# Kernel tuning notes

Measured on AMD Instinct MI355X. Metric: run time of the kernel, lower is better.

Reference implementation:

```python
import jax, jax.numpy as jnp
import numpy as np
import math

T, P, L, C, H, NPTS = 243, 17, 4, 128, 8, 4
DH = C // H


def _ln(x, g, b):
    m = jnp.mean(x, axis=-1, keepdims=True)
    v = jnp.mean((x - m) ** 2, axis=-1, keepdims=True)
    return (x - m) * jax.lax.rsqrt(v + 1e-5) * g + b


def _bilinear(v, grid):
    # v: [B, D, Hh, Ww]; grid: [B, Q, Pt, 2] in [-1,1], (x->W, y->H),
    # align_corners=False, zero padding (matches F.grid_sample in MSDeformAttn core)
    B, D, Hh, Ww = v.shape
    x = (grid[..., 0] + 1.0) * (Ww * 0.5) - 0.5
    y = (grid[..., 1] + 1.0) * (Hh * 0.5) - 0.5
    x0 = jnp.floor(x)
    y0 = jnp.floor(y)
    x0i = x0.astype(jnp.int32)
    y0i = y0.astype(jnp.int32)
    x1i = x0i + 1
    y1i = y0i + 1
    wx1 = x - x0
    wx0 = 1.0 - wx1
    wy1 = y - y0
    wy0 = 1.0 - wy1
    vf = v.reshape(B, D, Hh * Ww)
    Q, Pt = x.shape[1], x.shape[2]

    def gather(yi, xi):
        valid = ((yi >= 0) & (yi < Hh) & (xi >= 0) & (xi < Ww)).astype(v.dtype)
        idx = jnp.clip(yi, 0, Hh - 1) * Ww + jnp.clip(xi, 0, Ww - 1)
        g = jnp.take_along_axis(vf, idx.reshape(B, 1, Q * Pt), axis=2).reshape(B, D, Q, Pt)
        return g * valid[:, None]

    return (gather(y0i, x0i) * (wy0 * wx0)[:, None]
            + gather(y0i, x1i) * (wy0 * wx1)[:, None]
            + gather(y1i, x0i) * (wy1 * wx0)[:, None]
            + gather(y1i, x1i) * (wy1 * wx1)[:, None])  # [B, D, Q, Pt]


def _forward(x, ref_points, pe_buf, learn_pos, w_off, b_off, w_attn, b_attn,
             w_val, b_val, w_out, b_out, in_w, in_b, out_w, out_b,
             fc1_w, fc1_b, fc2_w, fc2_b, g1, be1, g2, be2, g3, be3):
    b, t, p, l, c = x.shape  # l = n_levels + 1
    Lq = t * p * L
    x0 = x[..., :1, :]
    xs = x[..., 1:, :].reshape(b, Lq, c)
    # --- subforward_self: norm_1 -> PE(query) -> MSDeformAttn ---
    xn = _ln(xs, g1, be1)
    q = (xn.reshape(b, t, p, L, c) + pe_buf + learn_pos).reshape(b, Lq, c)
    off = (q @ w_off.T + b_off).reshape(b, Lq, H, L, NPTS, 2)
    aw = jax.nn.softmax((q @ w_attn.T + b_attn).reshape(b, Lq, H, L * NPTS), axis=-1)
    aw = aw.reshape(b, Lq, H, L, NPTS)
    ref = jnp.broadcast_to(ref_points[:, :, :, None, :], (b, t, p, L, 2)).reshape(b, Lq, 2)
    normalizer = jnp.array([p, t], dtype=x.dtype)  # (W, H) per level
    loc = ref[:, :, None, None, None, :] + off / normalizer  # [b,Lq,H,L,Pt,2]
    grids = 2.0 * loc - 1.0
    val = (xn @ w_val.T + b_val).reshape(b, t, p, L, H, DH)
    v_maps = val.transpose(3, 0, 4, 5, 1, 2).reshape(L, b * H, DH, t, p)
    g = grids.transpose(3, 0, 2, 1, 4, 5).reshape(L, b * H, Lq, NPTS, 2)
    sampled = jax.vmap(_bilinear)(v_maps, g)  # [L, b*H, DH, Lq, Pt]
    aw_t = aw.transpose(3, 0, 2, 1, 4).reshape(L, b * H, 1, Lq, NPTS)
    o = jnp.sum(sampled * aw_t, axis=(0, 4))  # [b*H, DH, Lq]
    o = o.reshape(b, H, DH, Lq).transpose(0, 3, 1, 2).reshape(b, Lq, c)
    xs = (o @ w_out.T + b_out) + xs
    # --- concat level-0 back, cross (self) MHA over (p*l) tokens per frame ---
    xcat = jnp.concatenate([x0, xs.reshape(b, t, p, L, c)], axis=3).reshape(b * t, p * l, c)
    xn2 = _ln(xcat, g2, be2)
    qkv = xn2 @ in_w.T + in_b
    qh, kh, vh = jnp.split(qkv, 3, axis=-1)
    S = p * l
    qh = qh.reshape(b * t, S, H, DH)
    kh = kh.reshape(b * t, S, H, DH)
    vh = vh.reshape(b * t, S, H, DH)
    att = jax.nn.softmax(jnp.einsum('bqhd,bkhd->bhqk', qh, kh) / math.sqrt(DH), axis=-1)
    ca = jnp.einsum('bhqk,bkhd->bqhd', att, vh).reshape(b * t, S, c) @ out_w.T + out_b
    xcat = ca + xcat
    xr = xcat.reshape(b, t, p, l, c)
    # --- MLP block ---
    h = _ln(xr, g3, be3)
    h = jax.nn.gelu(h @ fc1_w.T + fc1_b, approximate=False) @ fc2_w.T + fc2_b
    return h + xr


def setup_inputs() -> dict:
    key = jax.random.key(0)
    ks = jax.random.split(key, 20)
    B = 2
    s = 0.02
    x = jax.random.normal(ks[0], (B, T, P, L + 1, C), jnp.float32)
    ref_points = jax.random.uniform(ks[1], (B, T, P, 2), dtype=jnp.float32)
    # sinusoidal PE buffer
    pos = np.arange(T, dtype=np.float32)[:, None]
    div = np.exp(np.arange(0, C, 2, dtype=np.float32) * (-math.log(10000.0) / C))
    ang = pos * div  # [T, C//2]
    pe = np.zeros((1, T, P, L, C), np.float32)
    pe[..., 0::2] = np.sin(ang)[None, :, None, None, :]
    pe[..., 1::2] = np.cos(ang)[None, :, None, None, :]
    rn = lambda k, shp: s * jax.random.normal(k, shp, jnp.float32)
    return {
        'x': x, 'ref_points': ref_points,
        'pe_buf': jnp.asarray(pe),
        'learn_pos': rn(ks[2], (1, T, P, L, C)),
        'w_off': rn(ks[3], (H * L * NPTS * 2, C)), 'b_off': rn(ks[4], (H * L * NPTS * 2,)),
        'w_attn': rn(ks[5], (H * L * NPTS, C)), 'b_attn': rn(ks[6], (H * L * NPTS,)),
        'w_val': rn(ks[7], (C, C)), 'b_val': rn(ks[8], (C,)),
        'w_out': rn(ks[9], (C, C)), 'b_out': rn(ks[10], (C,)),
        'in_w': rn(ks[11], (3 * C, C)), 'in_b': rn(ks[12], (3 * C,)),
        'out_w': rn(ks[13], (C, C)), 'out_b': rn(ks[14], (C,)),
        'fc1_w': rn(ks[15], (4 * C, C)), 'fc1_b': rn(ks[16], (4 * C,)),
        'fc2_w': rn(ks[17], (C, 4 * C)), 'fc2_b': rn(ks[18], (C,)),
        'g1': jnp.ones((C,), jnp.float32), 'be1': jnp.zeros((C,), jnp.float32),
        'g2': jnp.ones((C,), jnp.float32), 'be2': jnp.zeros((C,), jnp.float32),
        'g3': jnp.ones((C,), jnp.float32), 'be3': jnp.zeros((C,), jnp.float32),
    }


def reference(x, ref_points, pe_buf, learn_pos, w_off, b_off, w_attn, b_attn,
              w_val, b_val, w_out, b_out, in_w, in_b, out_w, out_b,
              fc1_w, fc1_b, fc2_w, fc2_b, g1, be1, g2, be2, g3, be3):
    return _forward(x, ref_points, pe_buf, learn_pos, w_off, b_off, w_attn, b_attn,
                    w_val, b_val, w_out, b_out, in_w, in_b, out_w, out_b,
                    fc1_w, fc1_b, fc2_w, fc2_b, g1, be1, g2, be2, g3, be3)
```

## Files before the change

### kernel.cpp

```cpp
#include <hip/hip_runtime.h>
#include <math.h>

#define T_ 243
#define P_ 17
#define L_ 4
#define C_ 128
#define H_ 8
#define NPTS_ 4
#define DH_ 16
#define B_ 2
#define LQ (T_*P_*L_)
#define NT1 (B_*LQ)
#define LL (L_+1)
#define S_ (P_*LL)
#define NT2 (B_*T_*P_*LL)

typedef __attribute__((ext_vector_type(8))) short short8v;
typedef __attribute__((ext_vector_type(4))) short short4v;
typedef __attribute__((ext_vector_type(4))) float float4v;

__device__ __forceinline__ unsigned short f2bf(float f){
  union { float f; unsigned u; } un; un.f = f;
  unsigned r = un.u + 0x7FFF + ((un.u >> 16) & 1);
  return (unsigned short)(r >> 16);
}
__device__ __forceinline__ float bf2f(unsigned short u){
  union { unsigned u; float f; } un; un.u = ((unsigned)u) << 16; return un.f;
}
__device__ __forceinline__ void dma16(const unsigned short* g, unsigned short* l){
  __builtin_amdgcn_global_load_lds(
      (const __attribute__((address_space(1))) void*)g,
      (__attribute__((address_space(3))) void*)l, 16, 0, 0);
}

__global__ void k_wcvt(const float* __restrict__ w0, const float* __restrict__ w1,
                       const float* __restrict__ w2, const float* __restrict__ w3,
                       const float* __restrict__ w4, const float* __restrict__ w5,
                       const float* __restrict__ w6, const float* __restrict__ w7,
                       unsigned short* __restrict__ dst){
  int i = blockIdx.x*256 + threadIdx.x;
  if (i >= 278528) return;
  float v;
  if      (i < 32768)  v = w0[i];
  else if (i < 49152)  v = w1[i-32768];
  else if (i < 65536)  v = w2[i-49152];
  else if (i < 81920)  v = w3[i-65536];
  else if (i < 131072) v = w4[i-81920];
  else if (i < 147456) v = w5[i-131072];
  else if (i < 212992) v = w6[i-147456];
  else                 v = w7[i-212992];
  dst[i] = f2bf(v);
}

__global__ __launch_bounds__(256) void k_ln1_q(
    const float* __restrict__ x, const float* __restrict__ pe,
    const float* __restrict__ lpos, const float* __restrict__ g1,
    const float* __restrict__ be1, const float* __restrict__ g2,
    const float* __restrict__ be2, unsigned short* __restrict__ xn,
    unsigned short* __restrict__ q, float* __restrict__ xcat,
    unsigned short* __restrict__ xn2) {
  int w = threadIdx.x >> 6; int lane = threadIdx.x & 63;
  int i = blockIdx.x*4 + w;
  int c = lane*2;
  if (i < NT1){
    int b = i / LQ; int r = i % LQ;
    int t = r / (P_*L_); int rp = r % (P_*L_);
    int p = rp / L_; int lv = rp % L_;
    const float* xrow = x + (((size_t)(b*T_+t)*P_ + p)*LL + 1 + lv)*C_;
    float2 v = *(const float2*)(xrow + c);
    float s1 = v.x + v.y, s2 = v.x*v.x + v.y*v.y;
    #pragma unroll
    for (int d=1; d<64; d<<=1){ s1 += __shfl_xor(s1,d); s2 += __shfl_xor(s2,d); }
    float mean = s1*(1.0f/C_);
    float var  = s2*(1.0f/C_) - mean*mean;
    float inv = rsqrtf(var + 1e-5f);
    float2 gg = *(const float2*)(g1 + c);
    float2 bb = *(const float2*)(be1 + c);
    float xn0 = (v.x - mean)*inv*gg.x + bb.x;
    float xn1 = (v.y - mean)*inv*gg.y + bb.y;
    size_t oi = (size_t)i*C_ + c;
    *(unsigned*)(xn + oi) = (unsigned)f2bf(xn0) | ((unsigned)f2bf(xn1) << 16);
    size_t pidx = (((size_t)t*P_ + p)*L_ + lv)*C_ + c;
    float2 pv = *(const float2*)(pe + pidx);
    float2 lp = *(const float2*)(lpos + pidx);
    *(unsigned*)(q + oi) = (unsigned)f2bf(xn0 + pv.x + lp.x) | ((unsigned)f2bf(xn1 + pv.y + lp.y) << 16);
  } else {
    int i0 = i - NT1;
    if (i0 >= B_*T_*P_) return;
    size_t xrow = (size_t)i0*LL;
    const float* xr = x + xrow*C_;
    float2 v = *(const float2*)(xr + c);
    float s1 = v.x + v.y, s2 = v.x*v.x + v.y*v.y;
    #pragma unroll
    for (int d=1; d<64; d<<=1){ s1 += __shfl_xor(s1,d); s2 += __shfl_xor(s2,d); }
    float mean = s1*(1.0f/C_);
    float var  = s2*(1.0f/C_) - mean*mean;
    float inv = rsqrtf(var + 1e-5f);
    float2 gg = *(const float2*)(g2 + c);
    float2 bb = *(const float2*)(be2 + c);
    *(float2*)(xcat + xrow*C_ + c) = v;
    float o0 = (v.x - mean)*inv*gg.x + bb.x;
    float o1 = (v.y - mean)*inv*gg.y + bb.y;
    *(unsigned*)(xn2 + xrow*C_ + c) = (unsigned)f2bf(o0) | ((unsigned)f2bf(o1) << 16);
  }
}

template<int K, int N, int EPI>
__global__ __launch_bounds__(256) void k_mm(
    const unsigned short* __restrict__ A, const unsigned short* __restrict__ Bw,
    const float* __restrict__ bias, const float* __restrict__ res,
    float* __restrict__ outF, unsigned short* __restrict__ outB,
    const float* __restrict__ xres, const float* __restrict__ lng,
    const float* __restrict__ lnbe, int M)
{
  constexpr int NST = K / 128;
  __shared__ unsigned short As[64*128];
  __shared__ unsigned short Bs[128*128];
  int tid = threadIdx.x;
  int lane = tid & 63;
  int w = tid >> 6;
  int lr = lane & 15, kg = lane >> 4;
  int m0 = blockIdx.x * 64;
  int n0 = blockIdx.y * 128;
  int lrow = lane >> 4;
  int lch  = lane & 15;
  float4v acc[8] = {};
  for (int st = 0; st < NST; ++st){
    int kk = st*128;
    if (st) __syncthreads();
    #pragma unroll
    for (int j = 0; j < 4; ++j){
      int rb = w*16 + j*4;
      int srcch = lch ^ ((rb + lrow) & 7);
      dma16(A + (size_t)(m0 + rb + lrow)*K + kk + srcch*8, As + rb*128);
    }
    #pragma unroll
    for (int j = 0; j < 8; ++j){
      int rb = w*32 + j*4;
      int srcch = lch ^ ((rb + lrow) & 7);
      dma16(Bw + (size_t)(n0 + rb + lrow)*K + kk + srcch*8, Bs + rb*128);
    }
    __syncthreads();
    #pragma unroll
    for (int ks = 0; ks < 4; ++ks){
      int cn = ks*4 + kg;
      int arow = w*16 + lr;
      short8v af = *(const short8v*)(As + arow*128 + ((cn ^ (arow & 7)) * 8));
      #pragma unroll
      for (int nf = 0; nf < 8; ++nf){
        int brow = nf*16 + lr;
        short8v bf = *(const short8v*)(Bs + brow*128 + ((cn ^ (brow & 7)) * 8));
        acc[nf] = __builtin_amdgcn_mfma_f32_16x16x32_bf16(af, bf, acc[nf], 0, 0, 0);
      }
    }
  }
  #pragma unroll
  for (int j = 0; j < 4; ++j){
    int gr = m0 + w*16 + kg*4 + j;
    if (gr >= M) continue;
    if (EPI == 3 || EPI == 4 || EPI == 5){
      #pragma unroll
      for (int nf = 0; nf < 8; ++nf){
        int gc = n0 + nf*16 + lr;
        float v = acc[nf][j] + bias[gc];
        if (EPI == 3) {
          outF[(size_t)gr*N + gc] = v + res[(size_t)gr*N + gc];
        } else if (EPI == 4) {
          float gv = 0.5f*v*(1.0f + erff(v*0.70710678118654752440f));
          outB[(size_t)gr*N + gc] = f2bf(gv);
        } else {
          outB[(size_t)gr*N + gc] = f2bf(v);
        }
      }
    } else {
      size_t xrow;
      if (EPI == 6){
        int b = gr / LQ; int r = gr % LQ;
        int t = r / (P_*L_); int rp = r % (P_*L_);
        int p = rp / L_; int lv = rp % L_;
        xrow = (((size_t)(b*T_+t)*P_ + p)*LL) + 1 + lv;
      } else {
        xrow = (size_t)gr;
      }
      float vals[8];
      float s = 0.f, sq = 0.f;
      #pragma unroll
      for (int nf = 0; nf < 8; ++nf){
        int gc = n0 + nf*16 + lr;
        float v = acc[nf][j] + bias[gc];
        if (EPI == 6) v += xres[xrow*C_ + gc];
        else          v += res[xrow*C_ + gc];
        vals[nf] = v; s += v; sq += v*v;
      }
      #pragma unroll
      for (int d = 1; d < 16; d <<= 1){ s += __shfl_xor(s, d); sq += __shfl_xor(sq, d); }
      float mean = s*(1.0f/128.f);
      float varr = sq*(1.0f/128.f) - mean*mean;
      float linv = rsqrtf(varr + 1e-5f);
      #pragma unroll
      for (int nf = 0; nf < 8; ++nf){
        int gc = n0 + nf*16 + lr;
        outF[xrow*C_ + gc] = vals[nf];
        float ln = (vals[nf] - mean)*linv*lng[gc] + lnbe[gc];
        outB[xrow*C_ + gc] = f2bf(ln);
      }
    }
  }
}

__global__ __launch_bounds__(256) void k_mm3(
    const unsigned short* __restrict__ Aq, const unsigned short* __restrict__ Axn,
    const unsigned short* __restrict__ Bw,
    const float* __restrict__ b_off, const float* __restrict__ b_attn,
    const float* __restrict__ b_val,
    unsigned short* __restrict__ off_b, unsigned short* __restrict__ aw_b,
    unsigned short* __restrict__ vm_b, int M)
{
  __shared__ unsigned short As[64*128];
  __shared__ unsigned short Bs[128*128];
  int tid = threadIdx.x;
  int lane = tid & 63;
  int w = tid >> 6;
  int lr = lane & 15, kg = lane >> 4;
  int m0 = blockIdx.x * 64;
  int y  = blockIdx.y;
  int n0 = y * 128;
  const unsigned short* A = (y == 3) ? Axn : Aq;
  int lrow = lane >> 4;
  int lch  = lane & 15;
  float4v acc[8] = {};
  #pragma unroll
  for (int j = 0; j < 4; ++j){
    int rb = w*16 + j*4;
    int srcch = lch ^ ((rb + lrow) & 7);
    dma16(A + (size_t)(m0 + rb + lrow)*128 + srcch*8, As + rb*128);
  }
  #pragma unroll
  for (int j = 0; j < 8; ++j){
    int rb = w*32 + j*4;
    int srcch = lch ^ ((rb + lrow) & 7);
    dma16(Bw + (size_t)(n0 + rb + lrow)*128 + srcch*8, Bs + rb*128);
  }
  __syncthreads();
  #pragma unroll
  for (int ks = 0; ks < 4; ++ks){
    int cn = ks*4 + kg;
    int arow = w*16 + lr;
    short8v af = *(const short8v*)(As + arow*128 + ((cn ^ (arow & 7)) * 8));
    #pragma unroll
    for (int nf = 0; nf < 8; ++nf){
      int brow = nf*16 + lr;
      short8v bf = *(const short8v*)(Bs + brow*128 + ((cn ^ (brow & 7)) * 8));
      acc[nf] = __builtin_amdgcn_mfma_f32_16x16x32_bf16(af, bf, acc[nf], 0, 0, 0);
    }
  }
  const float* bias = (y < 2) ? b_off : (y == 2 ? b_attn - 256 : b_val - 384);
  #pragma unroll
  for (int j = 0; j < 4; ++j){
    int gr = m0 + w*16 + kg*4 + j;
    if (gr >= M) continue;
    #pragma unroll
    for (int nf = 0; nf < 8; ++nf){
      int gc = n0 + nf*16 + lr;
      float v = acc[nf][j] + bias[gc];
      unsigned short bv = f2bf(v);
      if (y < 2)      off_b[(size_t)gr*256 + gc]       = bv;
      else if (y==2)  aw_b [(size_t)gr*128 + gc - 256] = bv;
      else            vm_b [(size_t)gr*128 + gc - 384] = bv;
    }
  }
}

__global__ __launch_bounds__(256) void k_sample(
    const unsigned short* __restrict__ off, const unsigned short* __restrict__ awl,
    const float* __restrict__ refp, const unsigned short* __restrict__ vmap,
    unsigned short* __restrict__ o){
  int gid = blockIdx.x*256 + threadIdx.x;
  if (gid >= NT1*H_) return;
  int h = gid & 7; int i = gid >> 3;
  int b = i / LQ; int r = i % LQ;
  int t = r/(P_*L_); int rp = r%(P_*L_); int p = rp/L_;
  size_t rpi = (((size_t)b*T_+t)*P_+p)*2;
  float refx = refp[rpi + 0]*P_ - 0.5f;
  float refy = refp[rpi + 1]*T_ - 0.5f;

  float offv[32];
  {
    const short8v* op8 = (const short8v*)(off + (size_t)i*256 + h*32);
    #pragma unroll
    for (int s=0;s<4;++s){ short8v v = op8[s];
      #pragma unroll
      for (int j=0;j<8;++j) offv[s*8+j] = bf2f((unsigned short)v[j]); }
  }
  float awv[16];
  {
    const short8v* ap8 = (const short8v*)(awl + (size_t)i*128 + h*16);
    #pragma unroll
    for (int s=0;s<2;++s){ short8v v = ap8[s];
      #pragma unroll
      for (int j=0;j<8;++j) awv[s*8+j] = bf2f((unsigned short)v[j]); }
  }
  float m = awv[0];
  #pragma unroll
  for (int k=1;k<16;++k) m = fmaxf(m, awv[k]);
  float sum = 0.f;
  #pragma unroll
  for (int k=0;k<16;++k){ awv[k] = __expf(awv[k]-m); sum += awv[k]; }
  float inv = 1.f/sum;
  #pragma unroll
  for (int k=0;k<16;++k) awv[k] *= inv;

  float acc[16];
  #pragma unroll
  for (int d=0;d<16;++d) acc[d]=0.f;

  #pragma unroll
  for (int lv=0; lv<L_; ++lv){
    const unsigned short* vlv = vmap + ((size_t)b*LQ + lv)*128 + h*16;
    #pragma unroll
    for (int pt=0; pt<NPTS_; ++pt){
      float px = refx + offv[(lv*4+pt)*2+0];
      float py = refy + offv[(lv*4+pt)*2+1];
      float w  = awv[lv*4+pt];
      float fx = floorf(px), fy = floorf(py);
      int x0 = (int)fx, y0 = (int)fy;
      float wx1 = px - fx, wx0 = 1.f - wx1;
      float wy1 = py - fy, wy0 = 1.f - wy1;
      float cw[4] = {w*wy0*wx0, w*wy0*wx1, w*wy1*wx0, w*wy1*wx1};
      int ys[4] = {y0, y0, y0+1, y0+1};
      int xs[4] = {x0, x0+1, x0, x0+1};
      #pragma unroll
      for (int cidx=0; cidx<4; ++cidx){
        int yy = ys[cidx], xx = xs[cidx];
        if (yy>=0 && yy<T_ && xx>=0 && xx<P_){
          const short8v* vp = (const short8v*)(vlv + (size_t)(yy*P_ + xx)*(L_*128));
          short8v v0 = vp[0], v1 = vp[1];
          float wgt = cw[cidx];
          #pragma unroll
          for (int d=0;d<8;++d){
            acc[d]   = fmaf(wgt, bf2f((unsigned short)v0[d]), acc[d]);
            acc[8+d] = fmaf(wgt, bf2f((unsigned short)v1[d]), acc[8+d]);
          }
        }
      }
    }
  }
  short8v o0, o1;
  #pragma unroll
  for (int d=0;d<8;++d){ o0[d] = (short)f2bf(acc[d]); o1[d] = (short)f2bf(acc[8+d]); }
  short8v* op = (short8v*)(o + (size_t)i*C_ + h*DH_);
  op[0] = o0; op[1] = o1;
}

#define AT6_WAVE 6976
__global__ __launch_bounds__(128) void k_attn6(const unsigned short* __restrict__ qkv,
                                               unsigned short* __restrict__ ca){
  __shared__ unsigned short alds[2*AT6_WAVE];
  int w = threadIdx.x >> 6; int lane = threadIdx.x & 63;
  int bt = blockIdx.x >> 2; int hp = blockIdx.x & 3;
  int h = hp*2 + w;
  unsigned short* Kb  = alds + w*AT6_WAVE;
  unsigned short* Vb  = Kb + 1920;
  unsigned short* Pb0 = Kb + 3648;
  unsigned short* Pb1 = Kb + 5312;
  const unsigned short* base = qkv + (size_t)bt*85*384 + h*16;
  for (int idx = lane; idx < 192; idx += 64){
    int s = idx >> 1; int d0 = (idx & 1)*8;
    short8v kv = {}, vv = {};
    if (s < 85){
      const unsigned short* rp = base + (size_t)s*384 + d0;
      kv = *(const short8v*)(rp + 128);
      vv = *(const short8v*)(rp + 256);
    }
    *(short8v*)(Kb + s*20 + d0) = kv;
    #pragma unroll
    for (int j=0;j<8;++j) Vb[(d0+j)*108 + s] = (unsigned short)vv[j];
  }
  __syncthreads();
  int g = lane >> 4; int li = lane & 15;
  const short8v zero8 = {};
  short8v qf0 = zero8, qf1 = zero8;
  if (g < 2){
    if (li < 85) qf0 = *(const short8v*)(base + (size_t)li*384 + g*8);
    int q1i = 16 + li;
    if (q1i < 85) qf1 = *(const short8v*)(base + (size_t)q1i*384 + g*8);
  }
  #pragma unroll 1
  for (int qp = 0; qp < 3; ++qp){
    short8v qn0 = zero8, qn1 = zero8;
    if (qp < 2 && g < 2){
      int a = (qp+1)*32 + li, b2 = a + 16;
      if (a  < 85) qn0 = *(const short8v*)(base + (size_t)a *384 + g*8);
      if (b2 < 85) qn1 = *(const short8v*)(base + (size_t)b2*384 + g*8);
    }
    float4v sc0[6], sc1[6];
    __builtin_amdgcn_s_setprio(1);
    #pragma unroll
    for (int kt = 0; kt < 6; ++kt){
      short8v kf = zero8;
      if (g < 2) kf = *(const short8v*)(Kb + (kt*16 + li)*20 + g*8);
      float4v z = {};
      sc0[kt] = __builtin_amdgcn_mfma_f32_16x16x32_bf16(kf, qf0, z, 0, 0, 0);
      sc1[kt] = __builtin_amdgcn_mfma_f32_16x16x32_bf16(kf, qf1, z, 0, 0, 0);
    }
    __builtin_amdgcn_s_setprio(0);
    float m0 = -1e30f, m1 = -1e30f;
    #pragma unroll
    for (int kt = 0; kt < 6; ++kt)
      #pragma unroll
      for (int j = 0; j < 4; ++j){
        bool msk = (kt == 5 && (g*4 + j) >= 5);
        float v0 = sc0[kt][j]*0.25f; if (msk) v0 = -1e30f;
        float v1 = sc1[kt][j]*0.25f; if (msk) v1 = -1e30f;
        sc0[kt][j] = v0; m0 = fmaxf(m0, v0);
        sc1[kt][j] = v1; m1 = fmaxf(m1, v1);
      }
    m0 = fmaxf(m0, __shfl_xor(m0, 16)); m1 = fmaxf(m1, __shfl_xor(m1, 16));
    m0 = fmaxf(m0, __shfl_xor(m0, 32)); m1 = fmaxf(m1, __shfl_xor(m1, 32));
    float sum0 = 0.f, sum1 = 0.f;
    #pragma unroll
    for (int kt = 0; kt < 6; ++kt){
      short4v p0, p1;
      #pragma unroll
      for (int j = 0; j < 4; ++j){
        float e0 = __expf(sc0[kt][j] - m0); sum0 += e0; p0[j] = (short)f2bf(e0);
        float e1 = __expf(sc1[kt][j] - m1); sum1 += e1; p1[j] = (short)f2bf(e1);
      }
      *(short4v*)(Pb0 + li*104 + kt*16 + g*4) = p0;
      *(short4v*)(Pb1 + li*104 + kt*16 + g*4) = p1;
    }
    sum0 += __shfl_xor(sum0, 16); sum1 += __shfl_xor(sum1, 16);
    sum0 += __shfl_xor(sum0, 32); sum1 += __shfl_xor(sum1, 32);
    float inv0 = 1.f/sum0, inv1 = 1.f/sum1;
    float4v o0 = {}, o1 = {};
    __builtin_amdgcn_s_setprio(1);
    #pragma unroll
    for (int kt32 = 0; kt32 < 3; ++kt32){
      short8v vf  = *(const short8v*)(Vb  + li*108 + kt32*32 + g*8);
      short8v p80 = *(const short8v*)(Pb0 + li*104 + kt32*32 + g*8);
      short8v p81 = *(const short8v*)(Pb1 + li*104 + kt32*32 + g*8);
      o0 = __builtin_amdgcn_mfma_f32_16x16x32_bf16(vf, p80, o0, 0, 0, 0);
      o1 = __builtin_amdgcn_mfma_f32_16x16x32_bf16(vf, p81, o1, 0, 0, 0);
    }
    __builtin_amdgcn_s_setprio(0);
    int q0 = qp*32 + li, q1 = q0 + 16;
    if (q0 < 85){
      short4v ov;
      #pragma unroll
      for (int j=0;j<4;++j) ov[j] = (short)f2bf(o0[j]*inv0);
      *(short4v*)(ca + ((size_t)bt*85 + q0)*128 + h*16 + g*4) = ov;
    }
    if (q1 < 85){
      short4v ov;
      #pragma unroll
      for (int j=0;j<4;++j) ov[j] = (short)f2bf(o1[j]*inv1);
      *(short4v*)(ca + ((size_t)bt*85 + q1)*128 + h*16 + g*4) = ov;
    }
    qf0 = qn0; qf1 = qn1;
  }
}

extern "C" void kernel_launch(void* const* d_in, const int* in_sizes, int n_in,
                              void* d_out, int out_size, void* d_ws, size_t ws_size,
                              hipStream_t stream) {
  (void)in_sizes; (void)n_in; (void)out_size; (void)ws_size;
  const float* x      = (const float*)d_in[0];
  const float* refp   = (const float*)d_in[1];
  const float* pe     = (const float*)d_in[2];
  const float* lpos   = (const float*)d_in[3];
  const float* w_off  = (const float*)d_in[4];
  const float* b_off  = (const float*)d_in[5];
  const float* w_attn = (const float*)d_in[6];
  const float* b_attn = (const float*)d_in[7];
  const float* w_val  = (const float*)d_in[8];
  const float* b_val  = (const float*)d_in[9];
  const float* w_out  = (const float*)d_in[10];
  const float* b_out  = (const float*)d_in[11];
  const float* in_w   = (const float*)d_in[12];
  const float* in_b   = (const float*)d_in[13];
  const float* out_w  = (const float*)d_in[14];
  const float* out_b  = (const float*)d_in[15];
  const float* fc1_w  = (const float*)d_in[16];
  const float* fc1_b  = (const float*)d_in[17];
  const float* fc2_w  = (const float*)d_in[18];
  const float* fc2_b  = (const float*)d_in[19];
  const float* g1     = (const float*)d_in[20];
  const float* be1    = (const float*)d_in[21];
  const float* g2     = (const float*)d_in[22];
  const float* be2    = (const float*)d_in[23];
  const float* g3     = (const float*)d_in[24];
  const float* be3    = (const float*)d_in[25];
  float* out = (float*)d_out;
  char* wsb = (char*)d_ws;

  unsigned short* xn_b  = (unsigned short*)(wsb + 0);
  unsigned short* q_b   = (unsigned short*)(wsb + 8460288);
  unsigned short* off_b = (unsigned short*)(wsb + 16920576);
  unsigned short* aw_b  = (unsigned short*)(wsb + 33841152);
  unsigned short* vm_b  = (unsigned short*)(wsb + 42301440);
  unsigned short* o_b   = (unsigned short*)(wsb + 50761728);
  float*          xcatB = (float*)(wsb + 59222016);
  unsigned short* xn2_b = (unsigned short*)(wsb + 80372736);
  unsigned short* qkv_b = (unsigned short*)(wsb + 90948096);
  unsigned short* wb    = (unsigned short*)(wsb + 122674176);
  unsigned short* ca_b  = (unsigned short*)(wsb + 0);
  unsigned short* ln3_b = (unsigned short*)(wsb + 80372736);
  unsigned short* hid_b = (unsigned short*)(wsb + 16920576);

  unsigned short* wb_off  = wb + 0;
  unsigned short* wb_wout = wb + 65536;
  unsigned short* wb_in   = wb + 81920;
  unsigned short* wb_outw = wb + 131072;
  unsigned short* wb_fc1  = wb + 147456;
  unsigned short* wb_fc2  = wb + 212992;

  const int GM1 = (NT1 + 63)/64;
  const int GM2 = (NT2 + 63)/64;

  hipLaunchKernelGGL(k_wcvt, dim3((278528+255)/256), dim3(256), 0, stream,
                     w_off, w_attn, w_val, w_out, in_w, out_w, fc1_w, fc2_w, wb);
  hipLaunchKernelGGL(k_ln1_q, dim3((NT1 + B_*T_*P_ + 3)/4), dim3(256), 0, stream,
                     x, pe, lpos, g1, be1, g2, be2, xn_b, q_b, xcatB, xn2_b);
  hipLaunchKernelGGL(k_mm3, dim3(GM1,4), dim3(256), 0, stream,
                     q_b, xn_b, wb_off, b_off, b_attn, b_val, off_b, aw_b, vm_b, NT1);
  hipLaunchKernelGGL(k_sample, dim3((NT1*H_+255)/256), dim3(256), 0, stream,
                     off_b, aw_b, refp, vm_b, o_b);
  hipLaunchKernelGGL((k_mm<128,128,6>), dim3(GM1,1), dim3(256), 0, stream,
                     o_b, wb_wout, b_out, nullptr, xcatB, xn2_b, x, g2, be2, NT1);
  hipLaunchKernelGGL((k_mm<128,384,5>), dim3(GM2,3), dim3(256), 0, stream,
                     xn2_b, wb_in, in_b, nullptr, nullptr, qkv_b, nullptr, nullptr, nullptr, NT2);
  hipLaunchKernelGGL(k_attn6, dim3(B_*T_*4), dim3(128), 0, stream, qkv_b, ca_b);
  hipLaunchKernelGGL((k_mm<128,128,7>), dim3(GM2,1), dim3(256), 0, stream,
                     ca_b, wb_outw, out_b, xcatB, xcatB, ln3_b, nullptr, g3, be3, NT2);
  hipLaunchKernelGGL((k_mm<128,512,4>), dim3(GM2,4), dim3(256), 0, stream,
                     ln3_b, wb_fc1, fc1_b, nullptr, nullptr, hid_b, nullptr, nullptr, nullptr, NT2);
  hipLaunchKernelGGL((k_mm<512,128,3>), dim3(GM2,1), dim3(256), 0, stream,
                     hid_b, wb_fc2, fc2_b, xcatB, out, nullptr, nullptr, nullptr, nullptr, NT2);
}
```

Measured before the change: 204.0 us.

## Fuse attention out-projection, LayerNorm3, FC1+GELU and FC2 into one FFN kernel

Result: slower. 216.6 us (+6.2%).

```diff
diff --git a/kernel.cpp b/kernel.cpp
--- a/kernel.cpp
+++ b/kernel.cpp
@@ -173,23 +173,17 @@
         }
       }
     } else {
-      size_t xrow;
-      if (EPI == 6){
-        int b = gr / LQ; int r = gr % LQ;
-        int t = r / (P_*L_); int rp = r % (P_*L_);
-        int p = rp / L_; int lv = rp % L_;
-        xrow = (((size_t)(b*T_+t)*P_ + p)*LL) + 1 + lv;
-      } else {
-        xrow = (size_t)gr;
-      }
+      int b = gr / LQ; int r = gr % LQ;
+      int t = r / (P_*L_); int rp = r % (P_*L_);
+      int p = rp / L_; int lv = rp % L_;
+      size_t xrow = (((size_t)(b*T_+t)*P_ + p)*LL) + 1 + lv;
       float vals[8];
       float s = 0.f, sq = 0.f;
       #pragma unroll
       for (int nf = 0; nf < 8; ++nf){
         int gc = n0 + nf*16 + lr;
         float v = acc[nf][j] + bias[gc];
-        if (EPI == 6) v += xres[xrow*C_ + gc];
-        else          v += res[xrow*C_ + gc];
+        v += xres[xrow*C_ + gc];
         vals[nf] = v; s += v; sq += v*v;
       }
       #pragma unroll
@@ -267,6 +261,145 @@
       if (y < 2)      off_b[(size_t)gr*256 + gc]       = bv;
       else if (y==2)  aw_b [(size_t)gr*128 + gc - 256] = bv;
       else            vm_b [(size_t)gr*128 + gc - 384] = bv;
+    }
+  }
+}
+
+__global__ __launch_bounds__(256) void k_ffn(
+    const unsigned short* __restrict__ ca, const unsigned short* __restrict__ wout,
+    const float* __restrict__ b_out, const float* __restrict__ xcat,
+    const float* __restrict__ g3, const float* __restrict__ be3,
+    const unsigned short* __restrict__ fc1w, const float* __restrict__ fc1b,
+    const unsigned short* __restrict__ fc2w, const float* __restrict__ fc2b,
+    float* __restrict__ out, int M)
+{
+  __shared__ unsigned short As[64*128];
+  __shared__ unsigned short Bs[128*128];
+  __shared__ unsigned short Hs[64*128];
+  int tid = threadIdx.x;
+  int lane = tid & 63;
+  int w = tid >> 6;
+  int lr = lane & 15, kg = lane >> 4;
+  int m0 = blockIdx.x * 64;
+  int lrow = lane >> 4;
+  int lch  = lane & 15;
+  #pragma unroll
+  for (int j = 0; j < 4; ++j){
+    int rb = w*16 + j*4;
+    int srcch = lch ^ ((rb + lrow) & 7);
+    dma16(ca + (size_t)(m0 + rb + lrow)*128 + srcch*8, As + rb*128);
+  }
+  #pragma unroll
+  for (int j = 0; j < 8; ++j){
+    int rb = w*32 + j*4;
+    int srcch = lch ^ ((rb + lrow) & 7);
+    dma16(wout + (size_t)(rb + lrow)*128 + srcch*8, Bs + rb*128);
+  }
+  __syncthreads();
+  float4v acc[8] = {};
+  #pragma unroll
+  for (int ks = 0; ks < 4; ++ks){
+    int cn = ks*4 + kg;
+    int arow = w*16 + lr;
+    short8v af = *(const short8v*)(As + arow*128 + ((cn ^ (arow & 7)) * 8));
+    #pragma unroll
+    for (int nf = 0; nf < 8; ++nf){
+      int brow = nf*16 + lr;
+      short8v bf = *(const short8v*)(Bs + brow*128 + ((cn ^ (brow & 7)) * 8));
+      acc[nf] = __builtin_amdgcn_mfma_f32_16x16x32_bf16(af, bf, acc[nf], 0, 0, 0);
+    }
+  }
+  __syncthreads();
+  float resv[4][8];
+  #pragma unroll
+  for (int j = 0; j < 4; ++j){
+    int gr = m0 + w*16 + kg*4 + j;
+    int lrow_o = w*16 + kg*4 + j;
+    float s = 0.f, sq = 0.f;
+    #pragma unroll
+    for (int nf = 0; nf < 8; ++nf){
+      int gc = nf*16 + lr;
+      float v = acc[nf][j] + b_out[gc] + xcat[(size_t)gr*C_ + gc];
+      resv[j][nf] = v; s += v; sq += v*v;
+    }
+    #pragma unroll
+    for (int d = 1; d < 16; d <<= 1){ s += __shfl_xor(s, d); sq += __shfl_xor(sq, d); }
+    float mean = s*(1.0f/128.f);
+    float varr = sq*(1.0f/128.f) - mean*mean;
+    float linv = rsqrtf(varr + 1e-5f);
+    #pragma unroll
+    for (int nf = 0; nf < 8; ++nf){
+      int gc = nf*16 + lr;
+      float ln = (resv[j][nf] - mean)*linv*g3[gc] + be3[gc];
+      int ch = (nf*2 + (lr>>3)) ^ (lrow_o & 7);
+      As[lrow_o*128 + ch*8 + (lr&7)] = f2bf(ln);
+    }
+  }
+  __syncthreads();
+  float4v acc2[8] = {};
+  for (int hc = 0; hc < 4; ++hc){
+    #pragma unroll
+    for (int j = 0; j < 8; ++j){
+      int rb = w*32 + j*4;
+      int srcch = lch ^ ((rb + lrow) & 7);
+      dma16(fc1w + (size_t)(hc*128 + rb + lrow)*128 + srcch*8, Bs + rb*128);
+    }
+    __syncthreads();
+    float4v a1[8] = {};
+    #pragma unroll
+    for (int ks = 0; ks < 4; ++ks){
+      int cn = ks*4 + kg;
+      int arow = w*16 + lr;
+      short8v af = *(const short8v*)(As + arow*128 + ((cn ^ (arow & 7)) * 8));
+      #pragma unroll
+      for (int nf = 0; nf < 8; ++nf){
+        int brow = nf*16 + lr;
+        short8v bf = *(const short8v*)(Bs + brow*128 + ((cn ^ (brow & 7)) * 8));
+        a1[nf] = __builtin_amdgcn_mfma_f32_16x16x32_bf16(af, bf, a1[nf], 0, 0, 0);
+      }
+    }
+    #pragma unroll
+    for (int j = 0; j < 4; ++j){
+      int lrow_o = w*16 + kg*4 + j;
+      #pragma unroll
+      for (int nf = 0; nf < 8; ++nf){
+        int gc = nf*16 + lr;
+        float v = a1[nf][j] + fc1b[hc*128 + gc];
+        float gv = 0.5f*v*(1.0f + erff(v*0.70710678118654752440f));
+        int ch = (nf*2 + (lr>>3)) ^ (lrow_o & 7);
+        Hs[lrow_o*128 + ch*8 + (lr&7)] = f2bf(gv);
+      }
+    }
+    __syncthreads();
+    #pragma unroll
+    for (int j = 0; j < 8; ++j){
+      int rb = w*32 + j*4;
+      int srcch = lch ^ ((rb + lrow) & 7);
+      dma16(fc2w + (size_t)(rb + lrow)*512 + hc*128 + srcch*8, Bs + rb*128);
+    }
+    __syncthreads();
+    #pragma unroll
+    for (int ks = 0; ks < 4; ++ks){
+      int cn = ks*4 + kg;
+      int arow = w*16 + lr;
+      short8v ah = *(const short8v*)(Hs + arow*128 + ((cn ^ (arow & 7)) * 8));
+      #pragma unroll
+      for (int nf = 0; nf < 8; ++nf){
+        int brow = nf*16 + lr;
+        short8v bh = *(const short8v*)(Bs + brow*128 + ((cn ^ (brow & 7)) * 8));
+        acc2[nf] = __builtin_amdgcn_mfma_f32_16x16x32_bf16(ah, bh, acc2[nf], 0, 0, 0);
+      }
+    }
+    __syncthreads();
+  }
+  #pragma unroll
+  for (int j = 0; j < 4; ++j){
+    int gr = m0 + w*16 + kg*4 + j;
+    if (gr >= M) continue;
+    #pragma unroll
+    for (int nf = 0; nf < 8; ++nf){
+      int gc = nf*16 + lr;
+      out[(size_t)gr*C_ + gc] = acc2[nf][j] + fc2b[gc] + resv[j][nf];
     }
   }
 }
@@ -504,8 +637,6 @@
   unsigned short* qkv_b = (unsigned short*)(wsb + 90948096);
   unsigned short* wb    = (unsigned short*)(wsb + 122674176);
   unsigned short* ca_b  = (unsigned short*)(wsb + 0);
-  unsigned short* ln3_b = (unsigned short*)(wsb + 80372736);
-  unsigned short* hid_b = (unsigned short*)(wsb + 16920576);
 
   unsigned short* wb_off  = wb + 0;
   unsigned short* wb_wout = wb + 65536;
@@ -530,10 +661,6 @@
   hipLaunchKernelGGL((k_mm<128,384,5>), dim3(GM2,3), dim3(256), 0, stream,
                      xn2_b, wb_in, in_b, nullptr, nullptr, qkv_b, nullptr, nullptr, nullptr, NT2);
   hipLaunchKernelGGL(k_attn6, dim3(B_*T_*4), dim3(128), 0, stream, qkv_b, ca_b);
-  hipLaunchKernelGGL((k_mm<128,128,7>), dim3(GM2,1), dim3(256), 0, stream,
-                     ca_b, wb_outw, out_b, xcatB, xcatB, ln3_b, nullptr, g3, be3, NT2);
-  hipLaunchKernelGGL((k_mm<128,512,4>), dim3(GM2,4), dim3(256), 0, stream,
-                     ln3_b, wb_fc1, fc1_b, nullptr, nullptr, hid_b, nullptr, nullptr, nullptr, NT2);
-  hipLaunchKernelGGL((k_mm<512,128,3>), dim3(GM2,1), dim3(256), 0, stream,
-                     hid_b, wb_fc2, fc2_b, xcatB, out, nullptr, nullptr, nullptr, nullptr, NT2);
-}
+  hipLaunchKernelGGL(k_ffn, dim3(GM2), dim3(256), 0, stream,
+                     ca_b, wb_outw, out_b, xcatB, g3, be3, wb_fc1, fc1_b, wb_fc2, fc2_b, out, NT2);
+}
```
